# Optimization experiments

Hardware: AMD Instinct MI355X
Metric: run time of the kernel (lower is better)

The kernel has to match this reference:

```python
import jax, jax.numpy as jnp
import numpy as np

B, S, D_MODEL, D_FF, NUM_EXPERTS, TOP_K = 2, 2048, 1024, 4096, 8, 2


def setup_inputs() -> dict:
    key = jax.random.key(0)
    ks = jax.random.split(key, 5)
    scale = 0.02
    return {
        "x": jax.random.normal(ks[0], (B, S, D_MODEL), jnp.float32),
        # gate: Linear(d_model, num_experts, bias=False); stored as [d_model, E]
        "Wg": jax.random.normal(ks[1], (D_MODEL, NUM_EXPERTS), jnp.float32) * scale,
        # stacked expert FFN params
        "W1": jax.random.normal(ks[2], (NUM_EXPERTS, D_MODEL, D_FF), jnp.float32) * scale,
        "b1": jnp.zeros((NUM_EXPERTS, D_FF), jnp.float32),
        "W2": jax.random.normal(ks[3], (NUM_EXPERTS, D_FF, D_MODEL), jnp.float32) * scale,
        "b2": jnp.zeros((NUM_EXPERTS, D_MODEL), jnp.float32),
    }


def _moe_forward(x, Wg, W1, b1, W2, b2):
    b, s, d = x.shape
    xt = x.reshape(-1, d)                       # [T, d]
    T = xt.shape[0]
    # --- TopKRouter ---
    probs = jax.nn.softmax(xt @ Wg, axis=-1)    # [T, E]
    w, idx = jax.lax.top_k(probs, TOP_K)        # [T, K]
    w = w / jnp.sum(w, axis=-1, keepdims=True)  # renormalize top-k weights
    # scatter routing weights into dense per-expert combine weights [T, E]
    gate = jnp.zeros((T, Wg.shape[1]), xt.dtype)
    gate = gate.at[jnp.arange(T)[:, None], idx].add(w)
    # --- per-expert FFN, weighted combine (scan over experts, E is small) ---
    def body(out, params):
        W1e, b1e, W2e, b2e, ge = params
        h = jax.nn.relu(xt @ W1e + b1e)         # [T, d_ff]
        out = out + (h @ W2e + b2e) * ge[:, None]
        return out, None
    out0 = jnp.zeros_like(xt)
    out, _ = jax.lax.scan(body, out0, (W1, b1, W2, b2, gate.T))
    return out.reshape(b, s, d)


def reference(x, Wg, W1, b1, W2, b2):
    # eval mode: dropout = identity, load-balance loss = None -> return output only
    return _moe_forward(x, Wg, W1, b1, W2, b2)
```

## Files before the change

kernel.cpp:

```cpp
#include <hip/hip_runtime.h>
#include <hip/hip_bf16.h>
#include <cstdint>
#include <cstddef>

#define T_TOK 4096
#define DM 1024
#define DFF 4096
#define NE 8
#define BT 128
#define BK 32
#define PADCAP (T_TOK * 2 + NE * BT)
#define MTILES (PADCAP / BT)

typedef __attribute__((ext_vector_type(8))) short short8;
typedef __attribute__((ext_vector_type(4))) float f32x4;

__device__ __forceinline__ unsigned short f2bf(float f) {
  unsigned int u = __float_as_uint(f);
  return (unsigned short)((u + 0x7fff + ((u >> 16) & 1)) >> 16);
}
__device__ __forceinline__ float bf2f(unsigned short u) {
  return __uint_as_float((unsigned int)u << 16);
}

__device__ __forceinline__ void load_lds16(const void* g, void* l) {
  __builtin_amdgcn_global_load_lds(
      (const __attribute__((address_space(1))) int*)g,
      (__attribute__((address_space(3))) int*)l, 16, 0, 0);
}

#define WAIT_VM4() __builtin_amdgcn_s_waitcnt(0x0F74)
#define WAIT_VM0() __builtin_amdgcn_s_waitcnt(0x0F70)
#define BARRIER()                          \
  do {                                     \
    __asm__ volatile("" ::: "memory");     \
    __builtin_amdgcn_s_barrier();          \
    __asm__ volatile("" ::: "memory");     \
  } while (0)

__global__ __launch_bounds__(256) void gate_kernel(
    const float* __restrict__ x, const float* __restrict__ Wg,
    int* __restrict__ counts, int* __restrict__ topk_idx,
    float* __restrict__ topk_w, unsigned short* __restrict__ xb) {
  int gid = blockIdx.x * blockDim.x + threadIdx.x;
  int t = gid >> 6;
  int lane = gid & 63;
  if (t >= T_TOK) return;
  const float* xr = x + (size_t)t * DM;
  unsigned short* xbr = xb + (size_t)t * DM;
  float acc[NE];
#pragma unroll
  for (int e = 0; e < NE; ++e) acc[e] = 0.f;
#pragma unroll
  for (int j = 0; j < DM / 64; ++j) {
    int d = lane + j * 64;
    float xv = xr[d];
    xbr[d] = f2bf(xv);
    const float4* wr = (const float4*)(Wg + (size_t)d * NE);
    float4 w0 = wr[0], w1 = wr[1];
    acc[0] += xv * w0.x; acc[1] += xv * w0.y;
    acc[2] += xv * w0.z; acc[3] += xv * w0.w;
    acc[4] += xv * w1.x; acc[5] += xv * w1.y;
    acc[6] += xv * w1.z; acc[7] += xv * w1.w;
  }
#pragma unroll
  for (int off = 32; off >= 1; off >>= 1) {
#pragma unroll
    for (int e = 0; e < NE; ++e) acc[e] += __shfl_xor(acc[e], off, 64);
  }
  if (lane == 0) {
    int i0 = 0;
#pragma unroll
    for (int e = 1; e < NE; ++e)
      if (acc[e] > acc[i0]) i0 = e;
    int i1 = (i0 == 0) ? 1 : 0;
#pragma unroll
    for (int e = 0; e < NE; ++e)
      if (e != i0 && acc[e] > acc[i1]) i1 = e;
    float e1 = __expf(acc[i1] - acc[i0]);
    float inv = 1.f / (1.f + e1);
    topk_idx[t * 2] = i0;
    topk_idx[t * 2 + 1] = i1;
    topk_w[t * 2] = inv;
    topk_w[t * 2 + 1] = e1 * inv;
    atomicAdd(&counts[i0], 1);
    atomicAdd(&counts[i1], 1);
  }
}

__global__ void init_kernel(int* counts, int* cursors, int* bucket_tok) {
  int i = blockIdx.x * blockDim.x + threadIdx.x;
  if (i < NE) { counts[i] = 0; cursors[i] = 0; }
  if (i < PADCAP) bucket_tok[i] = -1;
}

__global__ void offsets_kernel(const int* __restrict__ counts,
                               int* __restrict__ offsets) {
  if (threadIdx.x == 0) {
    int o = 0;
    offsets[0] = 0;
    for (int e = 0; e < NE; ++e) {
      o += (counts[e] + BT - 1) & ~(BT - 1);
      offsets[e + 1] = o;
    }
  }
}

__global__ void scatter_kernel(const int* __restrict__ topk_idx,
                               const int* __restrict__ offsets,
                               int* __restrict__ cursors,
                               int* __restrict__ bucket_tok,
                               int* __restrict__ slot_of) {
  int t = blockIdx.x * blockDim.x + threadIdx.x;
  if (t >= T_TOK) return;
#pragma unroll
  for (int k = 0; k < 2; ++k) {
    int e = topk_idx[t * 2 + k];
    int pos = atomicAdd(&cursors[e], 1);
    int slot = offsets[e] + pos;
    bucket_tok[slot] = t;
    slot_of[t * 2 + k] = slot;
  }
}

__global__ __launch_bounds__(256) void transpose_cvt_kernel(
    const float* __restrict__ W, unsigned short* __restrict__ Wt,
    int K, int N) {
  __shared__ float Ls[64][67];
  int e = blockIdx.z;
  const float* We = W + (size_t)e * K * N;
  unsigned short* Wte = Wt + (size_t)e * K * N;
  int k0 = blockIdx.x * 64, n0 = blockIdx.y * 64;
  int tid = threadIdx.x;
  int kr = tid >> 4, nf = (tid & 15) * 4;
#pragma unroll
  for (int p = 0; p < 4; ++p) {
    int k = kr + p * 16;
    float4 v = *(const float4*)(We + (size_t)(k0 + k) * N + n0 + nf);
    Ls[k][nf] = v.x; Ls[k][nf + 1] = v.y;
    Ls[k][nf + 2] = v.z; Ls[k][nf + 3] = v.w;
  }
  __syncthreads();
#pragma unroll
  for (int i = 0; i < 2; ++i) {
    int id = tid + i * 256;
    int n = id >> 3, kc = id & 7;
    short8 hv;
#pragma unroll
    for (int j = 0; j < 8; ++j) hv[j] = (short)f2bf(Ls[kc * 8 + j][n]);
    *(short8*)(Wte + (size_t)(n0 + n) * K + k0 + kc * 8) = hv;
  }
}


__global__ __launch_bounds__(256, 4) void gemm1_kernel(
    const unsigned short* __restrict__ xb, const unsigned short* __restrict__ Wt1,
    const float* __restrict__ b1, const int* __restrict__ offsets,
    const int* __restrict__ bucket_tok, unsigned short* __restrict__ h) {
  int r0 = blockIdx.x * BT;
  if (r0 >= offsets[NE]) return;
  int e = 0;
  while (offsets[e + 1] <= r0) ++e;
  int n0 = blockIdx.y * 128;

  __shared__ __align__(16) short As[2 * 128 * 32];
  __shared__ __align__(16) short Bs[2 * 128 * 32];
  __shared__ int toks[BT];

  int tid = threadIdx.x;
  if (tid < BT) toks[tid] = bucket_tok[r0 + tid];
  __syncthreads();

  int lane = tid & 63, w = tid >> 6;
  int rsub = lane >> 2, kc = lane & 3;
  int jsw = (kc ^ (rsub & 3)) * 8;
  const unsigned short* ga[2];
  const unsigned short* gb[2];
#pragma unroll
  for (int i = 0; i < 2; ++i) {
    int m = w * 32 + i * 16 + rsub;
    int tk = toks[m]; if (tk < 0) tk = 0;
    ga[i] = xb + (size_t)tk * DM + jsw;
    gb[i] = Wt1 + ((size_t)e * DFF + n0 + m) * DM + jsw;
  }
  int ldsW = w * 1024 + lane * 8;

  int wm = w & 1, wn = w >> 1;
  int g = lane >> 4, l15 = lane & 15;
  int cs = (g ^ (l15 & 3)) * 8;

  f32x4 acc[4][4];
#pragma unroll
  for (int i = 0; i < 4; ++i)
#pragma unroll
    for (int jj = 0; jj < 4; ++jj) acc[i][jj] = (f32x4){0.f, 0.f, 0.f, 0.f};

#pragma unroll
  for (int i = 0; i < 2; ++i) {
    load_lds16(ga[i], &As[ldsW + i * 512]);
    load_lds16(gb[i], &Bs[ldsW + i * 512]);
  }

  int buf = 0;
  const int NIT = DM / BK;
  for (int it = 0; it < NIT; ++it) {
    if (it + 1 < NIT) {
      int ko = (it + 1) * BK;
      int dst = (buf ^ 1) * 4096 + ldsW;
#pragma unroll
      for (int i = 0; i < 2; ++i) {
        load_lds16(ga[i] + ko, &As[dst + i * 512]);
        load_lds16(gb[i] + ko, &Bs[dst + i * 512]);
      }
      WAIT_VM4();
    } else {
      WAIT_VM0();
    }
    BARRIER();
    int bb = buf * 4096;
    short8 af[4], bfr[4];
#pragma unroll
    for (int mi = 0; mi < 4; ++mi)
      af[mi] = *(const short8*)&As[bb + (wm * 64 + mi * 16 + l15) * 32 + cs];
#pragma unroll
    for (int nj = 0; nj < 4; ++nj)
      bfr[nj] = *(const short8*)&Bs[bb + (wn * 64 + nj * 16 + l15) * 32 + cs];
#pragma unroll
    for (int mi = 0; mi < 4; ++mi)
#pragma unroll
      for (int nj = 0; nj < 4; ++nj)
        acc[mi][nj] = __builtin_amdgcn_mfma_f32_16x16x32_bf16(
            af[mi], bfr[nj], acc[mi][nj], 0, 0, 0);
    BARRIER();
    buf ^= 1;
  }

  unsigned short* wt =
      (unsigned short*)(w < 2 ? (void*)As : (void*)Bs) + (w & 1) * 4096;
  const float* b1e = b1 + (size_t)e * DFF;
#pragma unroll
  for (int nj = 0; nj < 4; ++nj) {
    int nl = nj * 16 + l15;
    float bv = b1e[n0 + wn * 64 + nl];
    int tchunk = nl >> 3, nin = nl & 7;
#pragma unroll
    for (int mi = 0; mi < 4; ++mi) {
#pragma unroll
      for (int r = 0; r < 4; ++r) {
        int ml = mi * 16 + g * 4 + r;
        float v = acc[mi][nj][r] + bv;
        wt[ml * 64 + (tchunk ^ (ml & 7)) * 8 + nin] = f2bf(fmaxf(v, 0.f));
      }
    }
  }
  int q = lane >> 3, c = lane & 7;
#pragma unroll
  for (int i = 0; i < 8; ++i) {
    int ml = i * 8 + q;
    short8 v = *(const short8*)&wt[ml * 64 + (c ^ (ml & 7)) * 8];
    *(short8*)(h + (size_t)(r0 + wm * 64 + ml) * DFF + n0 + wn * 64 + c * 8) = v;
  }
}

__global__ __launch_bounds__(256, 4) void gemm2_kernel(
    const unsigned short* __restrict__ h, const unsigned short* __restrict__ Wt2,
    const float* __restrict__ b2, const int* __restrict__ offsets,
    unsigned short* __restrict__ S) {
  int r0 = blockIdx.y * BT;
  if (r0 >= offsets[NE]) return;
  int e = 0;
  while (offsets[e + 1] <= r0) ++e;
  int n0 = (blockIdx.x & 7) * 128;
  int z = blockIdx.x >> 3;
  int kbeg = z * (DFF / 2);

  __shared__ __align__(16) short As[2 * 128 * 32];
  __shared__ __align__(16) short Bs[2 * 128 * 32];

  int tid = threadIdx.x;
  int lane = tid & 63, w = tid >> 6;
  int rsub = lane >> 2, kc = lane & 3;
  int jsw = (kc ^ (rsub & 3)) * 8;
  const unsigned short* ga[2];
  const unsigned short* gb[2];
#pragma unroll
  for (int i = 0; i < 2; ++i) {
    int m = w * 32 + i * 16 + rsub;
    ga[i] = h + ((size_t)(r0 + m)) * DFF + kbeg + jsw;
    gb[i] = Wt2 + ((size_t)e * DM + n0 + m) * DFF + kbeg + jsw;
  }
  int ldsW = w * 1024 + lane * 8;

  int wm = w & 1, wn = w >> 1;
  int g = lane >> 4, l15 = lane & 15;
  int cs = (g ^ (l15 & 3)) * 8;

  f32x4 acc[4][4];
#pragma unroll
  for (int i = 0; i < 4; ++i)
#pragma unroll
    for (int jj = 0; jj < 4; ++jj) acc[i][jj] = (f32x4){0.f, 0.f, 0.f, 0.f};

#pragma unroll
  for (int i = 0; i < 2; ++i) {
    load_lds16(ga[i], &As[ldsW + i * 512]);
    load_lds16(gb[i], &Bs[ldsW + i * 512]);
  }

  int buf = 0;
  const int NIT = (DFF / 2) / BK;
  for (int it = 0; it < NIT; ++it) {
    if (it + 1 < NIT) {
      int ko = (it + 1) * BK;
      int dst = (buf ^ 1) * 4096 + ldsW;
#pragma unroll
      for (int i = 0; i < 2; ++i) {
        load_lds16(ga[i] + ko, &As[dst + i * 512]);
        load_lds16(gb[i] + ko, &Bs[dst + i * 512]);
      }
      WAIT_VM4();
    } else {
      WAIT_VM0();
    }
    BARRIER();
    int bb = buf * 4096;
    short8 af[4], bfr[4];
#pragma unroll
    for (int mi = 0; mi < 4; ++mi)
      af[mi] = *(const short8*)&As[bb + (wm * 64 + mi * 16 + l15) * 32 + cs];
#pragma unroll
    for (int nj = 0; nj < 4; ++nj)
      bfr[nj] = *(const short8*)&Bs[bb + (wn * 64 + nj * 16 + l15) * 32 + cs];
#pragma unroll
    for (int mi = 0; mi < 4; ++mi)
#pragma unroll
      for (int nj = 0; nj < 4; ++nj)
        acc[mi][nj] = __builtin_amdgcn_mfma_f32_16x16x32_bf16(
            af[mi], bfr[nj], acc[mi][nj], 0, 0, 0);
    BARRIER();
    buf ^= 1;
  }

  unsigned short* wt =
      (unsigned short*)(w < 2 ? (void*)As : (void*)Bs) + (w & 1) * 4096;
  const float* b2e = b2 + (size_t)e * DM;
  float bscale = (z == 0) ? 1.f : 0.f;
  unsigned short* Sz = S + (size_t)z * PADCAP * DM;
#pragma unroll
  for (int nj = 0; nj < 4; ++nj) {
    int nl = nj * 16 + l15;
    float bv = b2e[n0 + wn * 64 + nl] * bscale;
    int tchunk = nl >> 3, nin = nl & 7;
#pragma unroll
    for (int mi = 0; mi < 4; ++mi) {
#pragma unroll
      for (int r = 0; r < 4; ++r) {
        int ml = mi * 16 + g * 4 + r;
        wt[ml * 64 + (tchunk ^ (ml & 7)) * 8 + nin] =
            f2bf(acc[mi][nj][r] + bv);
      }
    }
  }
  int q = lane >> 3, c = lane & 7;
#pragma unroll
  for (int i = 0; i < 8; ++i) {
    int ml = i * 8 + q;
    short8 v = *(const short8*)&wt[ml * 64 + (c ^ (ml & 7)) * 8];
    *(short8*)(Sz + (size_t)(r0 + wm * 64 + ml) * DM + n0 + wn * 64 + c * 8) =
        v;
  }
}

__global__ __launch_bounds__(256) void combine_kernel(
    const unsigned short* __restrict__ S, const int* __restrict__ slot_of,
    const float* __restrict__ topk_w, float* __restrict__ out) {
  int gid = blockIdx.x * 256 + threadIdx.x;
  int t = gid >> 7;
  int c = (gid & 127) * 8;
  int s0 = slot_of[t * 2], s1 = slot_of[t * 2 + 1];
  float w0 = topk_w[t * 2], w1 = topk_w[t * 2 + 1];
  const short8 a0 = *(const short8*)(S + (size_t)s0 * DM + c);
  const short8 a1 = *(const short8*)(S + ((size_t)PADCAP + s0) * DM + c);
  const short8 b0 = *(const short8*)(S + (size_t)s1 * DM + c);
  const short8 b1 = *(const short8*)(S + ((size_t)PADCAP + s1) * DM + c);
  float o[8];
#pragma unroll
  for (int j = 0; j < 8; ++j) {
    float va = bf2f((unsigned short)a0[j]) + bf2f((unsigned short)a1[j]);
    float vb = bf2f((unsigned short)b0[j]) + bf2f((unsigned short)b1[j]);
    o[j] = w0 * va + w1 * vb;
  }
  float* op = out + (size_t)t * DM + c;
  *(float4*)op = (float4){o[0], o[1], o[2], o[3]};
  *(float4*)(op + 4) = (float4){o[4], o[5], o[6], o[7]};
}

extern "C" void kernel_launch(void* const* d_in, const int* in_sizes, int n_in,
                              void* d_out, int out_size, void* d_ws,
                              size_t ws_size, hipStream_t stream) {
  const float* x = (const float*)d_in[0];
  const float* Wg = (const float*)d_in[1];
  const float* W1 = (const float*)d_in[2];
  const float* b1 = (const float*)d_in[3];
  const float* W2 = (const float*)d_in[4];
  const float* b2 = (const float*)d_in[5];
  float* out = (float*)d_out;

  int* ws_i = (int*)d_ws;
  int* counts = ws_i;
  int* offsets = ws_i + 8;
  int* cursors = ws_i + 20;
  int* bucket_tok = ws_i + 32;
  int* topk_idx = ws_i + 32 + PADCAP;
  float* topk_w = (float*)(ws_i + 32 + PADCAP + 2 * T_TOK);
  int* slot_of = ws_i + 32 + PADCAP + 4 * T_TOK;

  const size_t XB_OFF = 1u << 20;
  const size_t WT_OFF = XB_OFF + (size_t)T_TOK * DM * 2;
  const size_t H_OFF = WT_OFF + (size_t)NE * DM * DFF * 2;
  const size_t S_OFF = H_OFF + (size_t)PADCAP * DFF * 2;
  unsigned short* xb = (unsigned short*)((char*)d_ws + XB_OFF);
  unsigned short* Wt = (unsigned short*)((char*)d_ws + WT_OFF);
  unsigned short* h = (unsigned short*)((char*)d_ws + H_OFF);
  unsigned short* S = (unsigned short*)((char*)d_ws + S_OFF);

  init_kernel<<<(PADCAP + 255) / 256, 256, 0, stream>>>(counts, cursors,
                                                        bucket_tok);
  gate_kernel<<<T_TOK / 4, 256, 0, stream>>>(x, Wg, counts, topk_idx, topk_w,
                                             xb);
  offsets_kernel<<<1, 64, 0, stream>>>(counts, offsets);
  scatter_kernel<<<T_TOK / 256, 256, 0, stream>>>(topk_idx, offsets, cursors,
                                                  bucket_tok, slot_of);
  transpose_cvt_kernel<<<dim3(DM / 64, DFF / 64, NE), 256, 0, stream>>>(
      W1, Wt, DM, DFF);
  gemm1_kernel<<<dim3(MTILES, DFF / 128), 256, 0, stream>>>(
      xb, Wt, b1, offsets, bucket_tok, h);
  transpose_cvt_kernel<<<dim3(DFF / 64, DM / 64, NE), 256, 0, stream>>>(
      W2, Wt, DFF, DM);
  gemm2_kernel<<<dim3(16, MTILES), 256, 0, stream>>>(h, Wt, b2, offsets, S);
  combine_kernel<<<(T_TOK * DM / 8) / 256, 256, 0, stream>>>(S, slot_of,
                                                             topk_w, out);
}
```

Before: 720.0 us.

## Pre-swizzle weights into MFMA fragment layout and load B directly to registers

The weight transpose kernel now writes bf16 weights in a tiled layout that matches the MFMA B-fragment order, so both GEMMs can load B operands straight from global memory into registers instead of staging them through LDS. Only the activation tile stays in LDS, and BK doubles to 64 with a wider XOR swizzle. The gemm2 grid is transposed so consecutive blocks walk row tiles, and occupancy hints drop to 3 blocks per CU. The intent is to cut LDS traffic and barrier cost for the weight operand, at the price of more vector registers and exposed global-load latency on B.

New measurement: 684.2 us. -5.0%, faster.

```diff
diff --git a/kernel.cpp b/kernel.cpp
--- a/kernel.cpp
+++ b/kernel.cpp
@@ -8,7 +8,7 @@
 #define DFF 4096
 #define NE 8
 #define BT 128
-#define BK 32
+#define BK 64
 #define PADCAP (T_TOK * 2 + NE * BT)
 #define MTILES (PADCAP / BT)
 
@@ -31,6 +31,7 @@
 
 #define WAIT_VM4() __builtin_amdgcn_s_waitcnt(0x0F74)
 #define WAIT_VM0() __builtin_amdgcn_s_waitcnt(0x0F70)
+#define WAIT_LGKM0() __builtin_amdgcn_s_waitcnt(0xC07F)
 #define BARRIER()                          \
   do {                                     \
     __asm__ volatile("" ::: "memory");     \
@@ -129,7 +130,6 @@
   __shared__ float Ls[64][67];
   int e = blockIdx.z;
   const float* We = W + (size_t)e * K * N;
-  unsigned short* Wte = Wt + (size_t)e * K * N;
   int k0 = blockIdx.x * 64, n0 = blockIdx.y * 64;
   int tid = threadIdx.x;
   int kr = tid >> 4, nf = (tid & 15) * 4;
@@ -141,6 +141,7 @@
     Ls[k][nf + 2] = v.z; Ls[k][nf + 3] = v.w;
   }
   __syncthreads();
+  int KT = K >> 5, NT = N >> 4;
 #pragma unroll
   for (int i = 0; i < 2; ++i) {
     int id = tid + i * 256;
@@ -148,13 +149,16 @@
     short8 hv;
 #pragma unroll
     for (int j = 0; j < 8; ++j) hv[j] = (short)f2bf(Ls[kc * 8 + j][n]);
-    *(short8*)(Wte + (size_t)(n0 + n) * K + k0 + kc * 8) = hv;
-  }
-}
-
-
-__global__ __launch_bounds__(256, 4) void gemm1_kernel(
-    const unsigned short* __restrict__ xb, const unsigned short* __restrict__ Wt1,
+    size_t dst = (((size_t)e * KT + (k0 >> 5) + (kc >> 2)) * NT + (n0 >> 4) +
+                  (n >> 4)) * 512 +
+                 ((kc & 3) * 16 + (n & 15)) * 8;
+    *(short8*)(Wt + dst) = hv;
+  }
+}
+
+
+__global__ __launch_bounds__(256, 3) void gemm1_kernel(
+    const unsigned short* __restrict__ xb, const unsigned short* __restrict__ WtF,
     const float* __restrict__ b1, const int* __restrict__ offsets,
     const int* __restrict__ bucket_tok, unsigned short* __restrict__ h) {
   int r0 = blockIdx.x * BT;
@@ -163,8 +167,7 @@
   while (offsets[e + 1] <= r0) ++e;
   int n0 = blockIdx.y * 128;
 
-  __shared__ __align__(16) short As[2 * 128 * 32];
-  __shared__ __align__(16) short Bs[2 * 128 * 32];
+  __shared__ __align__(16) short LB[18432];
   __shared__ int toks[BT];
 
   int tid = threadIdx.x;
@@ -172,22 +175,22 @@
   __syncthreads();
 
   int lane = tid & 63, w = tid >> 6;
-  int rsub = lane >> 2, kc = lane & 3;
-  int jsw = (kc ^ (rsub & 3)) * 8;
-  const unsigned short* ga[2];
-  const unsigned short* gb[2];
-#pragma unroll
-  for (int i = 0; i < 2; ++i) {
-    int m = w * 32 + i * 16 + rsub;
+  int rr = lane >> 3, cc = lane & 7;
+  int jsw = (cc ^ (rr & 7)) * 8;
+  const unsigned short* ga[4];
+#pragma unroll
+  for (int i = 0; i < 4; ++i) {
+    int m = w * 32 + i * 8 + rr;
     int tk = toks[m]; if (tk < 0) tk = 0;
     ga[i] = xb + (size_t)tk * DM + jsw;
-    gb[i] = Wt1 + ((size_t)e * DFF + n0 + m) * DM + jsw;
-  }
-  int ldsW = w * 1024 + lane * 8;
+  }
+  int ldsW = w * 2048 + lane * 8;
 
   int wm = w & 1, wn = w >> 1;
   int g = lane >> 4, l15 = lane & 15;
-  int cs = (g ^ (l15 & 3)) * 8;
+  int x7 = l15 & 7;
+  const int KT = DM / 32, NT = DFF / 16;
+  size_t bbase = (((size_t)e * KT) * NT + (n0 >> 4) + wn * 4) * 512 + lane * 8;
 
   f32x4 acc[4][4];
 #pragma unroll
@@ -196,60 +199,61 @@
     for (int jj = 0; jj < 4; ++jj) acc[i][jj] = (f32x4){0.f, 0.f, 0.f, 0.f};
 
 #pragma unroll
-  for (int i = 0; i < 2; ++i) {
-    load_lds16(ga[i], &As[ldsW + i * 512]);
-    load_lds16(gb[i], &Bs[ldsW + i * 512]);
-  }
+  for (int i = 0; i < 4; ++i) load_lds16(ga[i], &LB[ldsW + i * 512]);
 
   int buf = 0;
   const int NIT = DM / BK;
   for (int it = 0; it < NIT; ++it) {
+    short8 bfr[2][4];
+#pragma unroll
+    for (int ks = 0; ks < 2; ++ks) {
+      size_t kb = bbase + (size_t)(it * 2 + ks) * NT * 512;
+#pragma unroll
+      for (int nj = 0; nj < 4; ++nj)
+        bfr[ks][nj] = *(const short8*)(WtF + kb + (size_t)nj * 512);
+    }
     if (it + 1 < NIT) {
       int ko = (it + 1) * BK;
-      int dst = (buf ^ 1) * 4096 + ldsW;
-#pragma unroll
-      for (int i = 0; i < 2; ++i) {
-        load_lds16(ga[i] + ko, &As[dst + i * 512]);
-        load_lds16(gb[i] + ko, &Bs[dst + i * 512]);
-      }
+      int dst = (buf ^ 1) * 8192 + ldsW;
+#pragma unroll
+      for (int i = 0; i < 4; ++i) load_lds16(ga[i] + ko, &LB[dst + i * 512]);
       WAIT_VM4();
     } else {
       WAIT_VM0();
     }
     BARRIER();
-    int bb = buf * 4096;
-    short8 af[4], bfr[4];
-#pragma unroll
-    for (int mi = 0; mi < 4; ++mi)
-      af[mi] = *(const short8*)&As[bb + (wm * 64 + mi * 16 + l15) * 32 + cs];
-#pragma unroll
-    for (int nj = 0; nj < 4; ++nj)
-      bfr[nj] = *(const short8*)&Bs[bb + (wn * 64 + nj * 16 + l15) * 32 + cs];
-#pragma unroll
-    for (int mi = 0; mi < 4; ++mi)
-#pragma unroll
-      for (int nj = 0; nj < 4; ++nj)
-        acc[mi][nj] = __builtin_amdgcn_mfma_f32_16x16x32_bf16(
-            af[mi], bfr[nj], acc[mi][nj], 0, 0, 0);
+    int bb = buf * 8192;
+#pragma unroll
+    for (int ks = 0; ks < 2; ++ks) {
+      short8 af[4];
+#pragma unroll
+      for (int mi = 0; mi < 4; ++mi)
+        af[mi] = *(const short8*)&LB[bb + (wm * 64 + mi * 16 + l15) * 64 +
+                                     (((ks * 4 + g) ^ x7)) * 8];
+#pragma unroll
+      for (int mi = 0; mi < 4; ++mi)
+#pragma unroll
+        for (int nj = 0; nj < 4; ++nj)
+          acc[mi][nj] = __builtin_amdgcn_mfma_f32_16x16x32_bf16(
+              af[mi], bfr[ks][nj], acc[mi][nj], 0, 0, 0);
+    }
+    WAIT_LGKM0();
     BARRIER();
     buf ^= 1;
   }
 
-  unsigned short* wt =
-      (unsigned short*)(w < 2 ? (void*)As : (void*)Bs) + (w & 1) * 4096;
+  short* wt = &LB[w * 4608];
   const float* b1e = b1 + (size_t)e * DFF;
 #pragma unroll
   for (int nj = 0; nj < 4; ++nj) {
     int nl = nj * 16 + l15;
     float bv = b1e[n0 + wn * 64 + nl];
-    int tchunk = nl >> 3, nin = nl & 7;
 #pragma unroll
     for (int mi = 0; mi < 4; ++mi) {
 #pragma unroll
       for (int r = 0; r < 4; ++r) {
         int ml = mi * 16 + g * 4 + r;
-        float v = acc[mi][nj][r] + bv;
-        wt[ml * 64 + (tchunk ^ (ml & 7)) * 8 + nin] = f2bf(fmaxf(v, 0.f));
+        wt[ml * 72 + nl] = (short)f2bf(fmaxf(acc[mi][nj][r] + bv, 0.f));
       }
     }
   }
@@ -257,43 +261,44 @@
 #pragma unroll
   for (int i = 0; i < 8; ++i) {
     int ml = i * 8 + q;
-    short8 v = *(const short8*)&wt[ml * 64 + (c ^ (ml & 7)) * 8];
+    short8 v = *(const short8*)&wt[ml * 72 + c * 8];
     *(short8*)(h + (size_t)(r0 + wm * 64 + ml) * DFF + n0 + wn * 64 + c * 8) = v;
   }
 }
 
-__global__ __launch_bounds__(256, 4) void gemm2_kernel(
-    const unsigned short* __restrict__ h, const unsigned short* __restrict__ Wt2,
+__global__ __launch_bounds__(256, 3) void gemm2_kernel(
+    const unsigned short* __restrict__ h, const unsigned short* __restrict__ WtF,
     const float* __restrict__ b2, const int* __restrict__ offsets,
     unsigned short* __restrict__ S) {
-  int r0 = blockIdx.y * BT;
+  int r0 = blockIdx.x * BT;
   if (r0 >= offsets[NE]) return;
   int e = 0;
   while (offsets[e + 1] <= r0) ++e;
-  int n0 = (blockIdx.x & 7) * 128;
-  int z = blockIdx.x >> 3;
+  int n0 = (blockIdx.y & 7) * 128;
+  int z = blockIdx.y >> 3;
   int kbeg = z * (DFF / 2);
 
-  __shared__ __align__(16) short As[2 * 128 * 32];
-  __shared__ __align__(16) short Bs[2 * 128 * 32];
+  __shared__ __align__(16) short LB[18432];
 
   int tid = threadIdx.x;
   int lane = tid & 63, w = tid >> 6;
-  int rsub = lane >> 2, kc = lane & 3;
-  int jsw = (kc ^ (rsub & 3)) * 8;
-  const unsigned short* ga[2];
-  const unsigned short* gb[2];
-#pragma unroll
-  for (int i = 0; i < 2; ++i) {
-    int m = w * 32 + i * 16 + rsub;
-    ga[i] = h + ((size_t)(r0 + m)) * DFF + kbeg + jsw;
-    gb[i] = Wt2 + ((size_t)e * DM + n0 + m) * DFF + kbeg + jsw;
-  }
-  int ldsW = w * 1024 + lane * 8;
+  int rr = lane >> 3, cc = lane & 7;
+  int jsw = (cc ^ (rr & 7)) * 8;
+  const unsigned short* ga[4];
+#pragma unroll
+  for (int i = 0; i < 4; ++i) {
+    int m = w * 32 + i * 8 + rr;
+    ga[i] = h + (size_t)(r0 + m) * DFF + kbeg + jsw;
+  }
+  int ldsW = w * 2048 + lane * 8;
 
   int wm = w & 1, wn = w >> 1;
   int g = lane >> 4, l15 = lane & 15;
-  int cs = (g ^ (l15 & 3)) * 8;
+  int x7 = l15 & 7;
+  const int KT = DFF / 32, NT = DM / 16;
+  size_t bbase =
+      (((size_t)e * KT + (kbeg >> 5)) * NT + (n0 >> 4) + wn * 4) * 512 +
+      lane * 8;
 
   f32x4 acc[4][4];
 #pragma unroll
@@ -302,47 +307,50 @@
     for (int jj = 0; jj < 4; ++jj) acc[i][jj] = (f32x4){0.f, 0.f, 0.f, 0.f};
 
 #pragma unroll
-  for (int i = 0; i < 2; ++i) {
-    load_lds16(ga[i], &As[ldsW + i * 512]);
-    load_lds16(gb[i], &Bs[ldsW + i * 512]);
-  }
+  for (int i = 0; i < 4; ++i) load_lds16(ga[i], &LB[ldsW + i * 512]);
 
   int buf = 0;
   const int NIT = (DFF / 2) / BK;
   for (int it = 0; it < NIT; ++it) {
+    short8 bfr[2][4];
+#pragma unroll
+    for (int ks = 0; ks < 2; ++ks) {
+      size_t kb = bbase + (size_t)(it * 2 + ks) * NT * 512;
+#pragma unroll
+      for (int nj = 0; nj < 4; ++nj)
+        bfr[ks][nj] = *(const short8*)(WtF + kb + (size_t)nj * 512);
+    }
     if (it + 1 < NIT) {
       int ko = (it + 1) * BK;
-      int dst = (buf ^ 1) * 4096 + ldsW;
-#pragma unroll
-      for (int i = 0; i < 2; ++i) {
-        load_lds16(ga[i] + ko, &As[dst + i * 512]);
-        load_lds16(gb[i] + ko, &Bs[dst + i * 512]);
-      }
+      int dst = (buf ^ 1) * 8192 + ldsW;
+#pragma unroll
+      for (int i = 0; i < 4; ++i) load_lds16(ga[i] + ko, &LB[dst + i * 512]);
       WAIT_VM4();
     } else {
       WAIT_VM0();
     }
     BARRIER();
-    int bb = buf * 4096;
-    short8 af[4], bfr[4];
-#pragma unroll
-    for (int mi = 0; mi < 4; ++mi)
-      af[mi] = *(const short8*)&As[bb + (wm * 64 + mi * 16 + l15) * 32 + cs];
-#pragma unroll
-    for (int nj = 0; nj < 4; ++nj)
-      bfr[nj] = *(const short8*)&Bs[bb + (wn * 64 + nj * 16 + l15) * 32 + cs];
-#pragma unroll
-    for (int mi = 0; mi < 4; ++mi)
-#pragma unroll
-      for (int nj = 0; nj < 4; ++nj)
-        acc[mi][nj] = __builtin_amdgcn_mfma_f32_16x16x32_bf16(
-            af[mi], bfr[nj], acc[mi][nj], 0, 0, 0);
+    int bb = buf * 8192;
+#pragma unroll
+    for (int ks = 0; ks < 2; ++ks) {
+      short8 af[4];
+#pragma unroll
+      for (int mi = 0; mi < 4; ++mi)
+        af[mi] = *(const short8*)&LB[bb + (wm * 64 + mi * 16 + l15) * 64 +
+                                     (((ks * 4 + g) ^ x7)) * 8];
+#pragma unroll
+      for (int mi = 0; mi < 4; ++mi)
+#pragma unroll
+        for (int nj = 0; nj < 4; ++nj)
+          acc[mi][nj] = __builtin_amdgcn_mfma_f32_16x16x32_bf16(
+              af[mi], bfr[ks][nj], acc[mi][nj], 0, 0, 0);
+    }
+    WAIT_LGKM0();
     BARRIER();
     buf ^= 1;
   }
 
-  unsigned short* wt =
-      (unsigned short*)(w < 2 ? (void*)As : (void*)Bs) + (w & 1) * 4096;
+  short* wt = &LB[w * 4608];
   const float* b2e = b2 + (size_t)e * DM;
   float bscale = (z == 0) ? 1.f : 0.f;
   unsigned short* Sz = S + (size_t)z * PADCAP * DM;
@@ -350,14 +358,12 @@
   for (int nj = 0; nj < 4; ++nj) {
     int nl = nj * 16 + l15;
     float bv = b2e[n0 + wn * 64 + nl] * bscale;
-    int tchunk = nl >> 3, nin = nl & 7;
 #pragma unroll
     for (int mi = 0; mi < 4; ++mi) {
 #pragma unroll
       for (int r = 0; r < 4; ++r) {
         int ml = mi * 16 + g * 4 + r;
-        wt[ml * 64 + (tchunk ^ (ml & 7)) * 8 + nin] =
-            f2bf(acc[mi][nj][r] + bv);
+        wt[ml * 72 + nl] = (short)f2bf(acc[mi][nj][r] + bv);
       }
     }
   }
@@ -365,7 +371,7 @@
 #pragma unroll
   for (int i = 0; i < 8; ++i) {
     int ml = i * 8 + q;
-    short8 v = *(const short8*)&wt[ml * 64 + (c ^ (ml & 7)) * 8];
+    short8 v = *(const short8*)&wt[ml * 72 + c * 8];
     *(short8*)(Sz + (size_t)(r0 + wm * 64 + ml) * DM + n0 + wn * 64 + c * 8) =
         v;
   }
@@ -437,7 +443,7 @@
       xb, Wt, b1, offsets, bucket_tok, h);
   transpose_cvt_kernel<<<dim3(DFF / 64, DM / 64, NE), 256, 0, stream>>>(
       W2, Wt, DFF, DM);
-  gemm2_kernel<<<dim3(16, MTILES), 256, 0, stream>>>(h, Wt, b2, offsets, S);
+  gemm2_kernel<<<dim3(MTILES, 16), 256, 0, stream>>>(h, Wt, b2, offsets, S);
   combine_kernel<<<(T_TOK * DM / 8) / 256, 256, 0, stream>>>(S, slot_of,
                                                              topk_w, out);
 }
```
